# Performance work log

Hardware: AMD Instinct MI355X
Metric: run time of the kernel (lower is better)

Reference implementation:

```python
import jax, jax.numpy as jnp
import numpy as np

B, S, D, H = 2, 2048, 1024, 16
DK = D // H


def setup_inputs() -> dict:
    key = jax.random.key(0)
    ks = jax.random.split(key, 11)
    scale = 1.0 / np.sqrt(D)
    inp = {
        "query": jax.random.normal(ks[0], (B, S, D), dtype=jnp.float32),
        "key": jax.random.normal(ks[1], (B, S, D), dtype=jnp.float32),
        "value": jax.random.normal(ks[2], (B, S, D), dtype=jnp.float32),
        "Wq": jax.random.normal(ks[3], (D, D), dtype=jnp.float32) * scale,
        "bq": jnp.zeros((D,), dtype=jnp.float32),
        "Wk": jax.random.normal(ks[4], (D, D), dtype=jnp.float32) * scale,
        "bk": jnp.zeros((D,), dtype=jnp.float32),
        "Wv": jax.random.normal(ks[5], (D, D), dtype=jnp.float32) * scale,
        "bv": jnp.zeros((D,), dtype=jnp.float32),
        "Wo": jax.random.normal(ks[6], (D, D), dtype=jnp.float32) * scale,
        "bo": jnp.zeros((D,), dtype=jnp.float32),
    }
    return inp


def _split_heads(x):
    # [B,S,D] -> [B,H,S,DK]
    b, s, _ = x.shape
    return x.reshape(b, s, H, DK).transpose(0, 2, 1, 3)


def reference(query, key, value, Wq, bq, Wk, bk, Wv, bv, Wo, bo):
    q = _split_heads(query @ Wq.T + bq)
    k = _split_heads(key @ Wk.T + bk)
    v = _split_heads(value @ Wv.T + bv)
    # scaled dot-product attention: [B,H,S,S]
    scores = jnp.einsum("bhqd,bhkd->bhqk", q, k) / np.sqrt(DK).astype(np.float32)
    attn = jax.nn.softmax(scores, axis=-1)  # stable max-subtract softmax, same math
    ctx = jnp.einsum("bhqk,bhkd->bhqd", attn, v)  # [B,H,S,DK]
    ctx = ctx.transpose(0, 2, 1, 3).reshape(query.shape[0], -1, H * DK)
    return ctx @ Wo.T + bo
```

## Files before the change

### kernel.cpp

```cpp
#include <hip/hip_runtime.h>
#include <math.h>

constexpr int NB = 2;
constexpr int NS = 2048;
constexpr int ND = 1024;
constexpr int NH = 16;
constexpr int NDK = 64;

typedef __attribute__((ext_vector_type(8))) short short8;
typedef __attribute__((ext_vector_type(4))) float floatx4;

__device__ inline unsigned short f2bf(float x) {
    unsigned u = __builtin_bit_cast(unsigned, x);
    u += 0x7fffu + ((u >> 16) & 1u);
    return (unsigned short)(u >> 16);
}

__device__ inline uint4 pack8(float4 a, float4 b) {
    unsigned short t[8] = {f2bf(a.x), f2bf(a.y), f2bf(a.z), f2bf(a.w),
                           f2bf(b.x), f2bf(b.y), f2bf(b.z), f2bf(b.w)};
    return *(uint4*)t;
}

#define GLOAD_LDS16(g, l) __builtin_amdgcn_global_load_lds( \
    (const __attribute__((address_space(1))) void*)(g),     \
    (__attribute__((address_space(3))) void*)(l), 16, 0, 0)

#define QSCALE 0.18033688f

__global__ __launch_bounds__(256) void cvt_all(
    const float* __restrict__ s0, const float* __restrict__ s1,
    const float* __restrict__ s2, const float* __restrict__ s3,
    const float* __restrict__ s4, const float* __restrict__ s5,
    const float* __restrict__ s6,
    unsigned short* __restrict__ d0, unsigned short* __restrict__ d1,
    unsigned short* __restrict__ d2, unsigned short* __restrict__ d3,
    unsigned short* __restrict__ d4, unsigned short* __restrict__ d5,
    unsigned short* __restrict__ d6)
{
    const int y = blockIdx.y;
    const float* srcs[7] = {s0, s1, s2, s3, s4, s5, s6};
    unsigned short* dsts[7] = {d0, d1, d2, d3, d4, d5, d6};
    const int nel = (y < 3) ? NB * NS * ND : ND * ND;
    int i = (blockIdx.x * 256 + threadIdx.x) * 8;
    if (i >= nel) return;
    const float* s = srcs[y];
    unsigned short* d = dsts[y];
    float4 a = *(const float4*)(s + i);
    float4 b = *(const float4*)(s + i + 4);
    *(uint4*)(d + i) = pack8(a, b);
}

template<int QA, int QB>
__device__ __forceinline__ void mfma_quad(
    floatx4 (&acc)[8][4], const short8 (&ta)[4][2], const short8 (&tb)[2][2][2])
{
#pragma unroll
    for (int ii = 0; ii < 4; ++ii)
#pragma unroll
        for (int jj = 0; jj < 2; ++jj) {
            acc[QA * 4 + ii][QB * 2 + jj] = __builtin_amdgcn_mfma_f32_16x16x32_bf16(
                ta[ii][0], tb[QB][jj][0], acc[QA * 4 + ii][QB * 2 + jj], 0, 0, 0);
            acc[QA * 4 + ii][QB * 2 + jj] = __builtin_amdgcn_mfma_f32_16x16x32_bf16(
                ta[ii][1], tb[QB][jj][1], acc[QA * 4 + ii][QB * 2 + jj], 0, 0, 0);
        }
}

__global__ __launch_bounds__(512, 2) void gemm_qkv(
    const unsigned short* __restrict__ Xq, const unsigned short* __restrict__ Xk,
    const unsigned short* __restrict__ Xv,
    const unsigned short* __restrict__ Wq, const unsigned short* __restrict__ Wk,
    const unsigned short* __restrict__ Wv,
    const float* __restrict__ bq, const float* __restrict__ bk,
    const float* __restrict__ bv,
    unsigned short* __restrict__ Cq, unsigned short* __restrict__ Ck,
    unsigned short* __restrict__ Cv)
{
    __shared__ unsigned short As[2][256 * 64];
    __shared__ unsigned short Bs[2][256 * 64];

    const int tid = threadIdx.x, w = tid >> 6, lane = tid & 63;
    const int lo = lane & 15, quad = lane >> 4;
    const int bid = blockIdx.x;
    const int seg = bid >> 6;
    const int idx = bid & 63;
    const int xcd = idx & 7;
    const int t8  = idx >> 3;
    const int K = ND;

    int bm, bn;
    const unsigned short *A, *Bw;
    const float* bias;
    if (seg == 2) {
        bm = t8 & 3; bn = (t8 >> 2) * 8 + xcd;
        A = Wv; Bw = Xv; bias = bv;
    } else {
        bn = t8 & 3; bm = (t8 >> 2) * 8 + xcd;
        if (seg == 1) { A = Xk; Bw = Wk; bias = bk; }
        else          { A = Xq; Bw = Wq; bias = bq; }
    }

    const int WM = (w >> 2) * 128, WN = (w & 3) * 64;

    const int srow = tid >> 3;
    const int sgo  = ((tid & 7) ^ (srow & 7)) * 8;
    const unsigned short* Asrc = A  + (size_t)(bm * 256 + srow) * K + sgo;
    const unsigned short* Bsrc = Bw + (size_t)(bn * 256 + srow) * K + sgo;

#define SA(bf_, t_, s_) GLOAD_LDS16(Asrc + (size_t)(s_) * 64 * K + (t_) * 64, \
                                    &As[bf_][(s_) * 4096 + tid * 8])
#define SB(bf_, t_, s_) GLOAD_LDS16(Bsrc + (size_t)(s_) * 64 * K + (t_) * 64, \
                                    &Bs[bf_][(s_) * 4096 + tid * 8])

    const int rp0 = ((quad) ^ (lo & 7)) * 8;
    const int rp1 = ((4 + quad) ^ (lo & 7)) * 8;

    short8 ta[4][2], tb[2][2][2];

#define RDA(bf_, qa_) { _Pragma("unroll") \
    for (int ii = 0; ii < 4; ++ii) { \
        const unsigned short* p_ = &As[bf_][(WM + (qa_) * 64 + ii * 16 + lo) * 64]; \
        ta[ii][0] = *(const short8*)(p_ + rp0); \
        ta[ii][1] = *(const short8*)(p_ + rp1); } }
#define RDB(bf_, qb_) { _Pragma("unroll") \
    for (int jj = 0; jj < 2; ++jj) { \
        const unsigned short* p_ = &Bs[bf_][(WN + (qb_) * 32 + jj * 16 + lo) * 64]; \
        tb[qb_][jj][0] = *(const short8*)(p_ + rp0); \
        tb[qb_][jj][1] = *(const short8*)(p_ + rp1); } }

#define PH_SYNC1 __builtin_amdgcn_s_barrier(); \
    asm volatile("s_waitcnt lgkmcnt(0)" ::: "memory"); \
    __builtin_amdgcn_sched_barrier(0); \
    __builtin_amdgcn_s_setprio(1);
#define PH_SYNC2 __builtin_amdgcn_s_setprio(0); \
    __builtin_amdgcn_sched_barrier(0); \
    __builtin_amdgcn_s_barrier();

    floatx4 acc[8][4];
#pragma unroll
    for (int i = 0; i < 8; ++i)
#pragma unroll
        for (int j = 0; j < 4; ++j) acc[i][j] = (floatx4){0.f, 0.f, 0.f, 0.f};

    SB(0, 0, 0); SB(0, 0, 1); SB(0, 0, 2); SB(0, 0, 3);
    SA(0, 0, 0); SA(0, 0, 1); SA(0, 0, 2); SA(0, 0, 3);
    SB(1, 1, 0); SB(1, 1, 1); SB(1, 1, 2); SB(1, 1, 3);
    asm volatile("s_waitcnt vmcnt(4)" ::: "memory");
    __builtin_amdgcn_s_barrier();

    constexpr int NIT = ND / 128;
#pragma unroll 1
    for (int it = 0; it < NIT; ++it) {
        const bool nl = (it < NIT - 1);
        const int t1 = 2 * it + 1, t2 = 2 * it + 2, t3 = 2 * it + 3;

        RDA(0, 0); RDB(0, 0);
        SA(1, t1, 0); SA(1, t1, 1);
        PH_SYNC1; mfma_quad<0, 0>(acc, ta, tb); PH_SYNC2;

        RDB(0, 1);
        SA(1, t1, 2); SA(1, t1, 3);
        PH_SYNC1; mfma_quad<0, 1>(acc, ta, tb); PH_SYNC2;

        RDA(0, 1);
        if (nl) { SB(0, t2, 0); SB(0, t2, 1); }
        PH_SYNC1; mfma_quad<1, 1>(acc, ta, tb); PH_SYNC2;

        if (nl) { SB(0, t2, 2); SB(0, t2, 3); }
        if (nl) asm volatile("s_waitcnt vmcnt(4)" ::: "memory");
        else    asm volatile("s_waitcnt vmcnt(0)" ::: "memory");
        PH_SYNC1; mfma_quad<1, 0>(acc, ta, tb); PH_SYNC2;

        RDA(1, 0); RDB(1, 0);
        if (nl) { SA(0, t2, 0); SA(0, t2, 1); }
        PH_SYNC1; mfma_quad<0, 0>(acc, ta, tb); PH_SYNC2;

        RDB(1, 1);
        if (nl) { SA(0, t2, 2); SA(0, t2, 3); }
        PH_SYNC1; mfma_quad<0, 1>(acc, ta, tb); PH_SYNC2;

        RDA(1, 1);
        if (nl) { SB(1, t3, 0); SB(1, t3, 1); }
        PH_SYNC1; mfma_quad<1, 1>(acc, ta, tb); PH_SYNC2;

        if (nl) { SB(1, t3, 2); SB(1, t3, 3); }
        if (nl) asm volatile("s_waitcnt vmcnt(4)" ::: "memory");
        PH_SYNC1; mfma_quad<1, 0>(acc, ta, tb); PH_SYNC2;
    }

#undef SA
#undef SB
#undef RDA
#undef RDB
#undef PH_SYNC1
#undef PH_SYNC2

    if (seg < 2) {
        unsigned short* C = seg ? Ck : Cq;
        const float scale = seg ? 1.f : QSCALE;
#pragma unroll
        for (int j = 0; j < 4; ++j) {
            const int col = bn * 256 + WN + j * 16 + lo;
            const float bb = bias[col];
#pragma unroll
            for (int i = 0; i < 8; ++i)
#pragma unroll
                for (int r = 0; r < 4; ++r) {
                    const int row = bm * 256 + WM + i * 16 + quad * 4 + r;
                    C[(size_t)row * ND + col] = f2bf((acc[i][j][r] + bb) * scale);
                }
        }
    } else {
#pragma unroll
        for (int i = 0; i < 8; ++i)
#pragma unroll
            for (int r = 0; r < 4; ++r) {
                const int row = bm * 256 + WM + i * 16 + quad * 4 + r;
                const float bb = bias[row];
#pragma unroll
                for (int j = 0; j < 4; ++j) {
                    const int col = bn * 256 + WN + j * 16 + lo;
                    const int b = col >> 11, s = col & (NS - 1);
                    Cv[(size_t)(b * ND + row) * NS + s] = f2bf(acc[i][j][r] + bb);
                }
            }
    }
}

constexpr int PRS = 72;

__global__ __launch_bounds__(512, 4) void attn_mfma(
    const unsigned short* __restrict__ qb,
    const unsigned short* __restrict__ kb,
    const unsigned short* __restrict__ vt,
    float* __restrict__ cacc0, float* __restrict__ cacc1,
    float* __restrict__ lbuf)
{
    __shared__ unsigned short Ks[2][64 * 64];
    __shared__ unsigned short Vs[2][64 * 64];
    __shared__ unsigned short Pt[8][32 * PRS];

    const int tid = threadIdx.x, w = tid >> 6, lane = tid & 63;
    const int lo = lane & 15, quad = lane >> 4;
    const int bid = blockIdx.x;
    const int xcd = bid & 7;
    const int tt  = bid >> 3;
    const int qgrp = tt & 7;
    const int bhk  = (tt >> 3) * 8 + xcd;
    const int bh = bhk >> 1, ksp = bhk & 1;
    const int b = bh >> 4, h = bh & 15;
    const int q0 = qgrp * 256 + w * 32;

    short8 qf[2][2];
    #pragma unroll
    for (int qt = 0; qt < 2; ++qt) {
        const unsigned short* qrow =
            qb + (size_t)(b * NS + q0 + qt * 16 + lo) * ND + h * NDK + quad * 8;
        qf[qt][0] = *(const short8*)(qrow);
        qf[qt][1] = *(const short8*)(qrow + 32);
    }

    const int r0 = tid >> 3, g0 = (tid & 7) ^ (r0 & 7);
    const unsigned short* Ksrc = kb + (size_t)(b * NS + r0) * ND + h * NDK + g0 * 8;
    const unsigned short* Vsrc = vt + (size_t)(bh * NDK + r0) * NS + g0 * 8;

#define STAGE(bf_, k_) { \
    GLOAD_LDS16(Ksrc + (size_t)(k_) * ND, &Ks[bf_][tid * 8]); \
    GLOAD_LDS16(Vsrc + (k_),              &Vs[bf_][tid * 8]); }

    floatx4 acc[2][4], lacc[2];
    #pragma unroll
    for (int qt = 0; qt < 2; ++qt) {
        lacc[qt] = (floatx4){0.f, 0.f, 0.f, 0.f};
        #pragma unroll
        for (int cb = 0; cb < 4; ++cb) acc[qt][cb] = (floatx4){0.f, 0.f, 0.f, 0.f};
    }

    const short8 ones = {0x3F80, 0x3F80, 0x3F80, 0x3F80,
                         0x3F80, 0x3F80, 0x3F80, 0x3F80};
    unsigned short* pw = &Pt[w][0];
    const int pos0 = (quad ^ (lo & 7)) * 8;
    const int pos1 = ((4 + quad) ^ (lo & 7)) * 8;

    const int kbase = ksp * 1024;
    STAGE(0, kbase);

    #pragma unroll 2
    for (int it = 0; it < 16; ++it) {
        const int bf = it & 1;
        if (it < 15) {
            STAGE(bf ^ 1, kbase + (it + 1) * 64);
            asm volatile("s_waitcnt vmcnt(2)" ::: "memory");
        } else {
            asm volatile("s_waitcnt vmcnt(0)" ::: "memory");
        }
        __builtin_amdgcn_s_barrier();
        __builtin_amdgcn_sched_barrier(0);

        const unsigned short* Kc = Ks[bf];
        const unsigned short* Vc = Vs[bf];

        floatx4 s[2][4];
        __builtin_amdgcn_s_setprio(1);
        #pragma unroll
        for (int t = 0; t < 4; ++t) {
            const int rw = (t * 16 + lo) * 64;
            const short8 kf0 = *(const short8*)(Kc + rw + pos0);
            const short8 kf1 = *(const short8*)(Kc + rw + pos1);
            #pragma unroll
            for (int qt = 0; qt < 2; ++qt) {
                s[qt][t] = __builtin_amdgcn_mfma_f32_16x16x32_bf16(
                    kf0, qf[qt][0], (floatx4){0.f, 0.f, 0.f, 0.f}, 0, 0, 0);
                s[qt][t] = __builtin_amdgcn_mfma_f32_16x16x32_bf16(
                    kf1, qf[qt][1], s[qt][t], 0, 0, 0);
            }
        }
        __builtin_amdgcn_s_setprio(0);

        #pragma unroll
        for (int qt = 0; qt < 2; ++qt)
            #pragma unroll
            for (int t = 0; t < 4; ++t) {
                unsigned u0 = __builtin_bit_cast(unsigned, __builtin_amdgcn_exp2f(s[qt][t][0]));
                unsigned u1 = __builtin_bit_cast(unsigned, __builtin_amdgcn_exp2f(s[qt][t][1]));
                unsigned u2 = __builtin_bit_cast(unsigned, __builtin_amdgcn_exp2f(s[qt][t][2]));
                unsigned u3 = __builtin_bit_cast(unsigned, __builtin_amdgcn_exp2f(s[qt][t][3]));
                uint2 pk = {(u0 >> 16) | (u1 & 0xFFFF0000u),
                            (u2 >> 16) | (u3 & 0xFFFF0000u)};
                *(uint2*)(pw + (qt * 16 + lo) * PRS + t * 16 + quad * 4) = pk;
            }

        short8 pf[2][2];
        #pragma unroll
        for (int qt = 0; qt < 2; ++qt) {
            pf[qt][0] = *(const short8*)(pw + (qt * 16 + lo) * PRS + quad * 8);
            pf[qt][1] = *(const short8*)(pw + (qt * 16 + lo) * PRS + 32 + quad * 8);
            lacc[qt] = __builtin_amdgcn_mfma_f32_16x16x32_bf16(pf[qt][0], ones, lacc[qt], 0, 0, 0);
            lacc[qt] = __builtin_amdgcn_mfma_f32_16x16x32_bf16(pf[qt][1], ones, lacc[qt], 0, 0, 0);
        }

        __builtin_amdgcn_s_setprio(1);
        #pragma unroll
        for (int cb = 0; cb < 4; ++cb) {
            const int rw = (cb * 16 + lo) * 64;
            const short8 vf0 = *(const short8*)(Vc + rw + pos0);
            const short8 vf1 = *(const short8*)(Vc + rw + pos1);
            #pragma unroll
            for (int qt = 0; qt < 2; ++qt) {
                acc[qt][cb] = __builtin_amdgcn_mfma_f32_16x16x32_bf16(pf[qt][0], vf0, acc[qt][cb], 0, 0, 0);
                acc[qt][cb] = __builtin_amdgcn_mfma_f32_16x16x32_bf16(pf[qt][1], vf1, acc[qt][cb], 0, 0, 0);
            }
        }
        __builtin_amdgcn_s_setprio(0);

        __builtin_amdgcn_sched_barrier(0);
        __builtin_amdgcn_s_barrier();
    }
#undef STAGE

    float* ca = ksp ? cacc1 : cacc0;
    float* lb = lbuf + (size_t)ksp * (NB * NH * NS);
    #pragma unroll
    for (int qt = 0; qt < 2; ++qt) {
        #pragma unroll
        for (int cb = 0; cb < 4; ++cb)
            #pragma unroll
            for (int r = 0; r < 4; ++r) {
                size_t off = (size_t)(b * NS + q0 + qt * 16 + quad * 4 + r) * ND
                           + h * NDK + cb * 16 + lo;
                ca[off] = acc[qt][cb][r];
            }
        if (lo == 0)
            #pragma unroll
            for (int r = 0; r < 4; ++r)
                lb[(size_t)bh * NS + q0 + qt * 16 + quad * 4 + r] = lacc[qt][r];
    }
}

__global__ __launch_bounds__(256) void gemm_o(
    const float* __restrict__ cacc0, const float* __restrict__ cacc1,
    const float* __restrict__ lbuf, const unsigned short* __restrict__ Bw,
    const float* __restrict__ bias, float* __restrict__ Cout)
{
    __shared__ unsigned short As[64 * 64];
    __shared__ unsigned short Bs[2][128 * 64];
    const int tid = threadIdx.x, w = tid >> 6, lane = tid & 63;
    const int lo = lane & 15, quad = lane >> 4;
    const int bid = blockIdx.x;
    const int xcd = bid & 7;
    const int tt  = bid >> 3;
    const int bn  = tt & 7;
    const int bm  = (tt >> 3) * 8 + xcd;
    const int K = ND;
    const int wm = (w >> 1) * 32, wn = (w & 1) * 64;
    const size_t LHALF = (size_t)NB * NH * NS;

    const int ar = tid >> 3;
    const int ag = (tid & 7) ^ (ar & 7);
    const int tok0 = bm * 64 + ar, tok1 = tok0 + 32;
    const float* A00 = cacc0 + (size_t)tok0 * ND + ag * 8;
    const float* A01 = cacc1 + (size_t)tok0 * ND + ag * 8;
    const float* A10 = cacc0 + (size_t)tok1 * ND + ag * 8;
    const float* A11 = cacc1 + (size_t)tok1 * ND + ag * 8;
    const size_t lb0 = (size_t)((tok0 >> 11) << 4) * NS + (tok0 & (NS - 1));
    const size_t lb1 = (size_t)((tok1 >> 11) << 4) * NS + (tok1 & (NS - 1));
    unsigned short* AsD0 = As + tid * 8;
    unsigned short* AsD1 = As + (tid + 256) * 8;

    const unsigned short* Bg[4];
    int bsoff[4];
    #pragma unroll
    for (int p = 0; p < 4; ++p) {
        int c = tid + 256 * p, r = c >> 3, g = (c & 7) ^ (r & 7);
        Bg[p] = Bw + (size_t)(bn * 128 + r) * K + g * 8;
        bsoff[p] = c * 8;
    }

    floatx4 acc[2][4];
    #pragma unroll
    for (int i = 0; i < 2; ++i)
        #pragma unroll
        for (int j = 0; j < 4; ++j) acc[i][j] = (floatx4){0.f, 0.f, 0.f, 0.f};

    #pragma unroll
    for (int p = 0; p < 4; ++p) GLOAD_LDS16(Bg[p], &Bs[0][bsoff[p]]);

    float4 ra[8];
    float lv0, lv1;
    ra[0] = *(const float4*)(A00);     ra[1] = *(const float4*)(A00 + 4);
    ra[2] = *(const float4*)(A01);     ra[3] = *(const float4*)(A01 + 4);
    ra[4] = *(const float4*)(A10);     ra[5] = *(const float4*)(A10 + 4);
    ra[6] = *(const float4*)(A11);     ra[7] = *(const float4*)(A11 + 4);
    lv0 = lbuf[lb0] + lbuf[lb0 + LHALF];
    lv1 = lbuf[lb1] + lbuf[lb1 + LHALF];

    #pragma unroll 1
    for (int t = 0; t < 16; ++t) {
        const int k0 = t * 64;
        const int cur = t & 1;
        if (t < 15) {
            #pragma unroll
            for (int p = 0; p < 4; ++p)
                GLOAD_LDS16(Bg[p] + k0 + 64, &Bs[cur ^ 1][bsoff[p]]);
        }
        const float inv0 = __builtin_amdgcn_rcpf(lv0);
        const float inv1 = __builtin_amdgcn_rcpf(lv1);
        if (t < 15) asm volatile("s_waitcnt vmcnt(4)" ::: "memory");
        else        asm volatile("s_waitcnt vmcnt(0)" ::: "memory");
        __builtin_amdgcn_s_barrier();
        __builtin_amdgcn_sched_barrier(0);

        {
            float4 s0 = {(ra[0].x + ra[2].x) * inv0, (ra[0].y + ra[2].y) * inv0,
                         (ra[0].z + ra[2].z) * inv0, (ra[0].w + ra[2].w) * inv0};
            float4 s1 = {(ra[1].x + ra[3].x) * inv0, (ra[1].y + ra[3].y) * inv0,
                         (ra[1].z + ra[3].z) * inv0, (ra[1].w + ra[3].w) * inv0};
            *(uint4*)AsD0 = pack8(s0, s1);
            float4 s2 = {(ra[4].x + ra[6].x) * inv1, (ra[4].y + ra[6].y) * inv1,
                         (ra[4].z + ra[6].z) * inv1, (ra[4].w + ra[6].w) * inv1};
            float4 s3 = {(ra[5].x + ra[7].x) * inv1, (ra[5].y + ra[7].y) * inv1,
                         (ra[5].z + ra[7].z) * inv1, (ra[5].w + ra[7].w) * inv1};
            *(uint4*)AsD1 = pack8(s2, s3);
        }

        if (t < 15) {
            const int kn = k0 + 64;
            ra[0] = *(const float4*)(A00 + kn); ra[1] = *(const float4*)(A00 + kn + 4);
            ra[2] = *(const float4*)(A01 + kn); ra[3] = *(const float4*)(A01 + kn + 4);
            ra[4] = *(const float4*)(A10 + kn); ra[5] = *(const float4*)(A10 + kn + 4);
            ra[6] = *(const float4*)(A11 + kn); ra[7] = *(const float4*)(A11 + kn + 4);
            const size_t hoff = (size_t)(kn >> 6) * NS;
            lv0 = lbuf[lb0 + hoff] + lbuf[lb0 + hoff + LHALF];
            lv1 = lbuf[lb1 + hoff] + lbuf[lb1 + hoff + LHALF];
        }

        asm volatile("s_waitcnt lgkmcnt(0)" ::: "memory");
        __builtin_amdgcn_sched_barrier(0);
        __builtin_amdgcn_s_barrier();

        __builtin_amdgcn_s_setprio(1);
        #pragma unroll
        for (int s = 0; s < 2; ++s) {
            const int pos = ((s * 4 + quad) ^ (lo & 7)) * 8;
            short8 af[2], bf[4];
            #pragma unroll
            for (int i = 0; i < 2; ++i)
                af[i] = *(const short8*)(As + (wm + i * 16 + lo) * 64 + pos);
            #pragma unroll
            for (int j = 0; j < 4; ++j)
                bf[j] = *(const short8*)(&Bs[cur][(wn + j * 16 + lo) * 64] + pos);
            #pragma unroll
            for (int i = 0; i < 2; ++i)
                #pragma unroll
                for (int j = 0; j < 4; ++j)
                    acc[i][j] = __builtin_amdgcn_mfma_f32_16x16x32_bf16(af[i], bf[j], acc[i][j], 0, 0, 0);
        }
        __builtin_amdgcn_s_setprio(0);
        __builtin_amdgcn_sched_barrier(0);
        __builtin_amdgcn_s_barrier();
    }

    #pragma unroll
    for (int j = 0; j < 4; ++j) {
        const int col = bn * 128 + wn + j * 16 + lo;
        const float bb = bias[col];
        #pragma unroll
        for (int i = 0; i < 2; ++i)
            #pragma unroll
            for (int r = 0; r < 4; ++r) {
                const int row = bm * 64 + wm + i * 16 + quad * 4 + r;
                Cout[(size_t)row * ND + col] = acc[i][j][r] + bb;
            }
    }
}

extern "C" void kernel_launch(void* const* d_in, const int* in_sizes, int n_in,
                              void* d_out, int out_size, void* d_ws, size_t ws_size,
                              hipStream_t stream)
{
    const float* query = (const float*)d_in[0];
    const float* key   = (const float*)d_in[1];
    const float* value = (const float*)d_in[2];
    const float* Wq    = (const float*)d_in[3];
    const float* bq    = (const float*)d_in[4];
    const float* Wk    = (const float*)d_in[5];
    const float* bk    = (const float*)d_in[6];
    const float* Wv    = (const float*)d_in[7];
    const float* bv    = (const float*)d_in[8];
    const float* Wo    = (const float*)d_in[9];
    const float* bo    = (const float*)d_in[10];
    float* out = (float*)d_out;

    const size_t n  = (size_t)NB * NS * ND;
    const size_t nw = (size_t)ND * ND;

    unsigned short* X0   = (unsigned short*)d_ws;
    unsigned short* X1   = X0 + n;
    unsigned short* X2   = X1 + n;
    unsigned short* W0   = X2 + n;
    unsigned short* W1   = W0 + nw;
    unsigned short* W2   = W1 + nw;
    unsigned short* W3   = W2 + nw;
    unsigned short* qbuf = W3 + nw;
    unsigned short* kbuf = qbuf + n;
    unsigned short* vtb  = kbuf + n;
    float* cacc1 = (float*)(vtb + n);
    float* lbuf  = cacc1 + n;
    float* cacc0 = (float*)X1;

    cvt_all<<<dim3((int)(n / 2048), 7), 256, 0, stream>>>(
        query, key, value, Wq, Wk, Wv, Wo, X0, X1, X2, W0, W1, W2, W3);

    gemm_qkv<<<192, 512, 0, stream>>>(X0, X1, X2, W0, W1, W2,
                                      bq, bk, bv, qbuf, kbuf, vtb);

    attn_mfma<<<512, 512, 0, stream>>>(qbuf, kbuf, vtb, cacc0, cacc1, lbuf);

    gemm_o<<<512, 256, 0, stream>>>(cacc0, cacc1, lbuf, W3, bo, out);
}
```

Before: 219.2 us.

## Triple-buffer K/V tiles with one barrier per iteration and swizzle P tile

Switches the attention K/V staging from double to triple buffering. The next-next tile is prefetched right after the barrier, which makes the trailing barrier unnecessary and halves the number of barriers per iteration. The padded P staging buffer (stride 72) is replaced by an unpadded 64-wide buffer with an XOR swizzle, to avoid LDS bank conflicts while using less shared memory. In exchange, LDS use for K/V goes up, which may limit occupancy at 4 blocks per CU, and the loop is no longer unrolled.

```diff
diff --git a/kernel.cpp b/kernel.cpp
--- a/kernel.cpp
+++ b/kernel.cpp
@@ -227,8 +227,6 @@
     }
 }
 
-constexpr int PRS = 72;
-
 __global__ __launch_bounds__(512, 4) void attn_mfma(
     const unsigned short* __restrict__ qb,
     const unsigned short* __restrict__ kb,
@@ -236,9 +234,9 @@
     float* __restrict__ cacc0, float* __restrict__ cacc1,
     float* __restrict__ lbuf)
 {
-    __shared__ unsigned short Ks[2][64 * 64];
-    __shared__ unsigned short Vs[2][64 * 64];
-    __shared__ unsigned short Pt[8][32 * PRS];
+    __shared__ unsigned short Ks[3][64 * 64];
+    __shared__ unsigned short Vs[3][64 * 64];
+    __shared__ unsigned short Pt[8][32 * 64];
 
     const int tid = threadIdx.x, w = tid >> 6, lane = tid & 63;
     const int lo = lane & 15, quad = lane >> 4;
@@ -263,10 +261,12 @@
     const int r0 = tid >> 3, g0 = (tid & 7) ^ (r0 & 7);
     const unsigned short* Ksrc = kb + (size_t)(b * NS + r0) * ND + h * NDK + g0 * 8;
     const unsigned short* Vsrc = vt + (size_t)(bh * NDK + r0) * NS + g0 * 8;
-
-#define STAGE(bf_, k_) { \
-    GLOAD_LDS16(Ksrc + (size_t)(k_) * ND, &Ks[bf_][tid * 8]); \
-    GLOAD_LDS16(Vsrc + (k_),              &Vs[bf_][tid * 8]); }
+    unsigned short* Ks0 = &Ks[0][0];
+    unsigned short* Vs0 = &Vs[0][0];
+
+#define STAGE(bi_, k_) { \
+    GLOAD_LDS16(Ksrc + (size_t)(k_) * ND, Ks0 + (bi_) * 4096 + tid * 8); \
+    GLOAD_LDS16(Vsrc + (k_),              Vs0 + (bi_) * 4096 + tid * 8); }
 
     floatx4 acc[2][4], lacc[2];
     #pragma unroll
@@ -281,24 +281,23 @@
     unsigned short* pw = &Pt[w][0];
     const int pos0 = (quad ^ (lo & 7)) * 8;
     const int pos1 = ((4 + quad) ^ (lo & 7)) * 8;
+    const int pxor = (lo & 7) << 3;
 
     const int kbase = ksp * 1024;
     STAGE(0, kbase);
-
-    #pragma unroll 2
+    STAGE(1, kbase + 64);
+
+    int rd = 0, wr = 2;
+    #pragma unroll 1
     for (int it = 0; it < 16; ++it) {
-        const int bf = it & 1;
-        if (it < 15) {
-            STAGE(bf ^ 1, kbase + (it + 1) * 64);
-            asm volatile("s_waitcnt vmcnt(2)" ::: "memory");
-        } else {
-            asm volatile("s_waitcnt vmcnt(0)" ::: "memory");
-        }
+        if (it < 15) asm volatile("s_waitcnt vmcnt(2)" ::: "memory");
+        else         asm volatile("s_waitcnt vmcnt(0)" ::: "memory");
         __builtin_amdgcn_s_barrier();
         __builtin_amdgcn_sched_barrier(0);
-
-        const unsigned short* Kc = Ks[bf];
-        const unsigned short* Vc = Vs[bf];
+        if (it < 14) STAGE(wr, kbase + (it + 2) * 64);
+
+        const unsigned short* Kc = Ks0 + rd * 4096;
+        const unsigned short* Vc = Vs0 + rd * 4096;
 
         floatx4 s[2][4];
         __builtin_amdgcn_s_setprio(1);
@@ -327,14 +326,14 @@
                 unsigned u3 = __builtin_bit_cast(unsigned, __builtin_amdgcn_exp2f(s[qt][t][3]));
                 uint2 pk = {(u0 >> 16) | (u1 & 0xFFFF0000u),
                             (u2 >> 16) | (u3 & 0xFFFF0000u)};
-                *(uint2*)(pw + (qt * 16 + lo) * PRS + t * 16 + quad * 4) = pk;
+                *(uint2*)(pw + (qt * 16 + lo) * 64 + ((t * 16 + quad * 4) ^ pxor)) = pk;
             }
 
         short8 pf[2][2];
         #pragma unroll
         for (int qt = 0; qt < 2; ++qt) {
-            pf[qt][0] = *(const short8*)(pw + (qt * 16 + lo) * PRS + quad * 8);
-            pf[qt][1] = *(const short8*)(pw + (qt * 16 + lo) * PRS + 32 + quad * 8);
+            pf[qt][0] = *(const short8*)(pw + (qt * 16 + lo) * 64 + pos0);
+            pf[qt][1] = *(const short8*)(pw + (qt * 16 + lo) * 64 + pos1);
             lacc[qt] = __builtin_amdgcn_mfma_f32_16x16x32_bf16(pf[qt][0], ones, lacc[qt], 0, 0, 0);
             lacc[qt] = __builtin_amdgcn_mfma_f32_16x16x32_bf16(pf[qt][1], ones, lacc[qt], 0, 0, 0);
         }
@@ -353,8 +352,8 @@
         }
         __builtin_amdgcn_s_setprio(0);
 
-        __builtin_amdgcn_sched_barrier(0);
-        __builtin_amdgcn_s_barrier();
+        rd = (rd == 2) ? 0 : rd + 1;
+        wr = (wr == 2) ? 0 : wr + 1;
     }
 #undef STAGE
 
```

New measurement: 217.7 us (median of 2 runs). Within noise of the previous version (-0.7%).

## Fuse fp32-to-bf16 conversion into QKV GEMM loads, drop separate convert pass

Applied to the files above, without the earlier changes.

The QKV projection GEMM now reads fp32 activations and weights directly from global memory into registers, converts them to bf16 and writes them into LDS. Previously a separate kernel converted all inputs to bf16 first, and the GEMM used async global-to-LDS loads. Only the Wo weight is still converted by a small standalone kernel. This removes one full read and write pass over the inputs and one kernel launch. In exchange the GEMM loads twice the bytes per tile, the stages sync on register loads instead of async LDS DMA, and register pressure rises.

```diff
diff --git a/kernel.cpp b/kernel.cpp
--- a/kernel.cpp
+++ b/kernel.cpp
@@ -28,24 +28,10 @@
 
 #define QSCALE 0.18033688f
 
-__global__ __launch_bounds__(256) void cvt_all(
-    const float* __restrict__ s0, const float* __restrict__ s1,
-    const float* __restrict__ s2, const float* __restrict__ s3,
-    const float* __restrict__ s4, const float* __restrict__ s5,
-    const float* __restrict__ s6,
-    unsigned short* __restrict__ d0, unsigned short* __restrict__ d1,
-    unsigned short* __restrict__ d2, unsigned short* __restrict__ d3,
-    unsigned short* __restrict__ d4, unsigned short* __restrict__ d5,
-    unsigned short* __restrict__ d6)
+__global__ __launch_bounds__(256) void cvt_w(
+    const float* __restrict__ s, unsigned short* __restrict__ d)
 {
-    const int y = blockIdx.y;
-    const float* srcs[7] = {s0, s1, s2, s3, s4, s5, s6};
-    unsigned short* dsts[7] = {d0, d1, d2, d3, d4, d5, d6};
-    const int nel = (y < 3) ? NB * NS * ND : ND * ND;
     int i = (blockIdx.x * 256 + threadIdx.x) * 8;
-    if (i >= nel) return;
-    const float* s = srcs[y];
-    unsigned short* d = dsts[y];
     float4 a = *(const float4*)(s + i);
     float4 b = *(const float4*)(s + i + 4);
     *(uint4*)(d + i) = pack8(a, b);
@@ -67,10 +53,10 @@
 }
 
 __global__ __launch_bounds__(512, 2) void gemm_qkv(
-    const unsigned short* __restrict__ Xq, const unsigned short* __restrict__ Xk,
-    const unsigned short* __restrict__ Xv,
-    const unsigned short* __restrict__ Wq, const unsigned short* __restrict__ Wk,
-    const unsigned short* __restrict__ Wv,
+    const float* __restrict__ Xq, const float* __restrict__ Xk,
+    const float* __restrict__ Xv,
+    const float* __restrict__ Wq, const float* __restrict__ Wk,
+    const float* __restrict__ Wv,
     const float* __restrict__ bq, const float* __restrict__ bk,
     const float* __restrict__ bv,
     unsigned short* __restrict__ Cq, unsigned short* __restrict__ Ck,
@@ -89,7 +75,7 @@
     const int K = ND;
 
     int bm, bn;
-    const unsigned short *A, *Bw;
+    const float *A, *Bw;
     const float* bias;
     if (seg == 2) {
         bm = t8 & 3; bn = (t8 >> 2) * 8 + xcd;
@@ -104,13 +90,15 @@
 
     const int srow = tid >> 3;
     const int sgo  = ((tid & 7) ^ (srow & 7)) * 8;
-    const unsigned short* Asrc = A  + (size_t)(bm * 256 + srow) * K + sgo;
-    const unsigned short* Bsrc = Bw + (size_t)(bn * 256 + srow) * K + sgo;
-
-#define SA(bf_, t_, s_) GLOAD_LDS16(Asrc + (size_t)(s_) * 64 * K + (t_) * 64, \
-                                    &As[bf_][(s_) * 4096 + tid * 8])
-#define SB(bf_, t_, s_) GLOAD_LDS16(Bsrc + (size_t)(s_) * 64 * K + (t_) * 64, \
-                                    &Bs[bf_][(s_) * 4096 + tid * 8])
+    const float* Asrc = A  + (size_t)(bm * 256 + srow) * K + sgo;
+    const float* Bsrc = Bw + (size_t)(bn * 256 + srow) * K + sgo;
+
+#define LDA(t_, s_, a_, b_) { const float* p_ = Asrc + (size_t)(s_) * 64 * K + (t_) * 64; \
+    a_ = *(const float4*)(p_); b_ = *(const float4*)(p_ + 4); }
+#define LDB(t_, s_, a_, b_) { const float* p_ = Bsrc + (size_t)(s_) * 64 * K + (t_) * 64; \
+    a_ = *(const float4*)(p_); b_ = *(const float4*)(p_ + 4); }
+#define WRA(bf_, s_, a_, b_) *(uint4*)(&As[bf_][(s_) * 4096 + tid * 8]) = pack8(a_, b_);
+#define WRB(bf_, s_, a_, b_) *(uint4*)(&Bs[bf_][(s_) * 4096 + tid * 8]) = pack8(a_, b_);
 
     const int rp0 = ((quad) ^ (lo & 7)) * 8;
     const int rp1 = ((4 + quad) ^ (lo & 7)) * 8;
@@ -128,11 +116,14 @@
         tb[qb_][jj][0] = *(const short8*)(p_ + rp0); \
         tb[qb_][jj][1] = *(const short8*)(p_ + rp1); } }
 
-#define PH_SYNC1 __builtin_amdgcn_s_barrier(); \
+#define PH_IN  __builtin_amdgcn_sched_barrier(0); \
+    __builtin_amdgcn_s_barrier(); \
     asm volatile("s_waitcnt lgkmcnt(0)" ::: "memory"); \
     __builtin_amdgcn_sched_barrier(0); \
     __builtin_amdgcn_s_setprio(1);
-#define PH_SYNC2 __builtin_amdgcn_s_setprio(0); \
+#define PH_MID __builtin_amdgcn_s_setprio(0); \
+    __builtin_amdgcn_sched_barrier(0);
+#define PH_OUT asm volatile("s_waitcnt lgkmcnt(0)" ::: "memory"); \
     __builtin_amdgcn_sched_barrier(0); \
     __builtin_amdgcn_s_barrier();
 
@@ -142,11 +133,17 @@
 #pragma unroll
         for (int j = 0; j < 4; ++j) acc[i][j] = (floatx4){0.f, 0.f, 0.f, 0.f};
 
-    SB(0, 0, 0); SB(0, 0, 1); SB(0, 0, 2); SB(0, 0, 3);
-    SA(0, 0, 0); SA(0, 0, 1); SA(0, 0, 2); SA(0, 0, 3);
-    SB(1, 1, 0); SB(1, 1, 1); SB(1, 1, 2); SB(1, 1, 3);
-    asm volatile("s_waitcnt vmcnt(4)" ::: "memory");
-    __builtin_amdgcn_s_barrier();
+    {
+        float4 f0, f1, f2, f3, f4, f5, f6, f7;
+        LDB(0, 0, f0, f1); LDB(0, 1, f2, f3); LDB(0, 2, f4, f5); LDB(0, 3, f6, f7);
+        WRB(0, 0, f0, f1); WRB(0, 1, f2, f3); WRB(0, 2, f4, f5); WRB(0, 3, f6, f7);
+        LDA(0, 0, f0, f1); LDA(0, 1, f2, f3); LDA(0, 2, f4, f5); LDA(0, 3, f6, f7);
+        WRA(0, 0, f0, f1); WRA(0, 1, f2, f3); WRA(0, 2, f4, f5); WRA(0, 3, f6, f7);
+        LDB(1, 0, f0, f1); LDB(1, 1, f2, f3); LDB(1, 2, f4, f5); LDB(1, 3, f6, f7);
+        WRB(1, 0, f0, f1); WRB(1, 1, f2, f3); WRB(1, 2, f4, f5); WRB(1, 3, f6, f7);
+        asm volatile("s_waitcnt lgkmcnt(0)" ::: "memory");
+        __builtin_amdgcn_s_barrier();
+    }
 
     constexpr int NIT = ND / 128;
 #pragma unroll 1
@@ -154,46 +151,79 @@
         const bool nl = (it < NIT - 1);
         const int t1 = 2 * it + 1, t2 = 2 * it + 2, t3 = 2 * it + 3;
 
-        RDA(0, 0); RDB(0, 0);
-        SA(1, t1, 0); SA(1, t1, 1);
-        PH_SYNC1; mfma_quad<0, 0>(acc, ta, tb); PH_SYNC2;
-
-        RDB(0, 1);
-        SA(1, t1, 2); SA(1, t1, 3);
-        PH_SYNC1; mfma_quad<0, 1>(acc, ta, tb); PH_SYNC2;
-
-        RDA(0, 1);
-        if (nl) { SB(0, t2, 0); SB(0, t2, 1); }
-        PH_SYNC1; mfma_quad<1, 1>(acc, ta, tb); PH_SYNC2;
-
-        if (nl) { SB(0, t2, 2); SB(0, t2, 3); }
-        if (nl) asm volatile("s_waitcnt vmcnt(4)" ::: "memory");
-        else    asm volatile("s_waitcnt vmcnt(0)" ::: "memory");
-        PH_SYNC1; mfma_quad<1, 0>(acc, ta, tb); PH_SYNC2;
-
-        RDA(1, 0); RDB(1, 0);
-        if (nl) { SA(0, t2, 0); SA(0, t2, 1); }
-        PH_SYNC1; mfma_quad<0, 0>(acc, ta, tb); PH_SYNC2;
-
-        RDB(1, 1);
-        if (nl) { SA(0, t2, 2); SA(0, t2, 3); }
-        PH_SYNC1; mfma_quad<0, 1>(acc, ta, tb); PH_SYNC2;
-
-        RDA(1, 1);
-        if (nl) { SB(1, t3, 0); SB(1, t3, 1); }
-        PH_SYNC1; mfma_quad<1, 1>(acc, ta, tb); PH_SYNC2;
-
-        if (nl) { SB(1, t3, 2); SB(1, t3, 3); }
-        if (nl) asm volatile("s_waitcnt vmcnt(4)" ::: "memory");
-        PH_SYNC1; mfma_quad<1, 0>(acc, ta, tb); PH_SYNC2;
-    }
-
-#undef SA
-#undef SB
+        {
+            float4 f0, f1, f2, f3;
+            RDA(0, 0); RDB(0, 0);
+            LDA(t1, 0, f0, f1); LDA(t1, 1, f2, f3);
+            PH_IN; mfma_quad<0, 0>(acc, ta, tb); PH_MID;
+            WRA(1, 0, f0, f1); WRA(1, 1, f2, f3);
+            PH_OUT;
+        }
+        {
+            float4 f0, f1, f2, f3;
+            RDB(0, 1);
+            LDA(t1, 2, f0, f1); LDA(t1, 3, f2, f3);
+            PH_IN; mfma_quad<0, 1>(acc, ta, tb); PH_MID;
+            WRA(1, 2, f0, f1); WRA(1, 3, f2, f3);
+            PH_OUT;
+        }
+        {
+            float4 f0, f1, f2, f3;
+            RDA(0, 1);
+            if (nl) { LDB(t2, 0, f0, f1); LDB(t2, 1, f2, f3); }
+            PH_IN; mfma_quad<1, 1>(acc, ta, tb); PH_MID;
+            if (nl) { WRB(0, 0, f0, f1); WRB(0, 1, f2, f3); }
+            PH_OUT;
+        }
+        {
+            float4 f0, f1, f2, f3;
+            if (nl) { LDB(t2, 2, f0, f1); LDB(t2, 3, f2, f3); }
+            PH_IN; mfma_quad<1, 0>(acc, ta, tb); PH_MID;
+            if (nl) { WRB(0, 2, f0, f1); WRB(0, 3, f2, f3); }
+            PH_OUT;
+        }
+        {
+            float4 f0, f1, f2, f3;
+            RDA(1, 0); RDB(1, 0);
+            if (nl) { LDA(t2, 0, f0, f1); LDA(t2, 1, f2, f3); }
+            PH_IN; mfma_quad<0, 0>(acc, ta, tb); PH_MID;
+            if (nl) { WRA(0, 0, f0, f1); WRA(0, 1, f2, f3); }
+            PH_OUT;
+        }
+        {
+            float4 f0, f1, f2, f3;
+            RDB(1, 1);
+            if (nl) { LDA(t2, 2, f0, f1); LDA(t2, 3, f2, f3); }
+            PH_IN; mfma_quad<0, 1>(acc, ta, tb); PH_MID;
+            if (nl) { WRA(0, 2, f0, f1); WRA(0, 3, f2, f3); }
+            PH_OUT;
+        }
+        {
+            float4 f0, f1, f2, f3;
+            RDA(1, 1);
+            if (nl) { LDB(t3, 0, f0, f1); LDB(t3, 1, f2, f3); }
+            PH_IN; mfma_quad<1, 1>(acc, ta, tb); PH_MID;
+            if (nl) { WRB(1, 0, f0, f1); WRB(1, 1, f2, f3); }
+            PH_OUT;
+        }
+        {
+            float4 f0, f1, f2, f3;
+            if (nl) { LDB(t3, 2, f0, f1); LDB(t3, 3, f2, f3); }
+            PH_IN; mfma_quad<1, 0>(acc, ta, tb); PH_MID;
+            if (nl) { WRB(1, 2, f0, f1); WRB(1, 3, f2, f3); }
+            PH_OUT;
+        }
+    }
+
+#undef LDA
+#undef LDB
+#undef WRA
+#undef WRB
 #undef RDA
 #undef RDB
-#undef PH_SYNC1
-#undef PH_SYNC2
+#undef PH_IN
+#undef PH_MID
+#undef PH_OUT
 
     if (seg < 2) {
         unsigned short* C = seg ? Ck : Cq;
@@ -548,10 +578,9 @@
     float* lbuf  = cacc1 + n;
     float* cacc0 = (float*)X1;
 
-    cvt_all<<<dim3((int)(n / 2048), 7), 256, 0, stream>>>(
-        query, key, value, Wq, Wk, Wv, Wo, X0, X1, X2, W0, W1, W2, W3);
-
-    gemm_qkv<<<192, 512, 0, stream>>>(X0, X1, X2, W0, W1, W2,
+    cvt_w<<<512, 256, 0, stream>>>(Wo, W3);
+
+    gemm_qkv<<<192, 512, 0, stream>>>(query, key, value, Wq, Wk, Wv,
                                       bq, bk, bv, qbuf, kbuf, vtb);
 
     attn_mfma<<<512, 512, 0, stream>>>(qbuf, kbuf, vtb, cacc0, cacc1, lbuf);
```

Measured after the change: 397.4 us. +81.3%, slower.

## Halve attention query tile per wave and double grid with XOR-swizzled P buffer

Applied to the files above, without the earlier changes.

Each wave of the attention kernel now handles 16 query rows instead of 32, so a block covers 128 queries and the grid doubles to 1024 blocks. The P staging buffer drops its padded stride for an XOR swizzle, and launch bounds ask for 6 blocks per CU. The aim is more parallelism and occupancy through lower register and LDS use. In exchange, each K/V tile loaded into LDS is reused by half as many queries, so K/V global traffic doubles.

```diff
diff --git a/kernel.cpp b/kernel.cpp
--- a/kernel.cpp
+++ b/kernel.cpp
@@ -227,9 +227,7 @@
     }
 }
 
-constexpr int PRS = 72;
-
-__global__ __launch_bounds__(512, 4) void attn_mfma(
+__global__ __launch_bounds__(512, 6) void attn_mfma(
     const unsigned short* __restrict__ qb,
     const unsigned short* __restrict__ kb,
     const unsigned short* __restrict__ vt,
@@ -238,26 +236,25 @@
 {
     __shared__ unsigned short Ks[2][64 * 64];
     __shared__ unsigned short Vs[2][64 * 64];
-    __shared__ unsigned short Pt[8][32 * PRS];
+    __shared__ unsigned short Pt[8][16 * 64];
 
     const int tid = threadIdx.x, w = tid >> 6, lane = tid & 63;
     const int lo = lane & 15, quad = lane >> 4;
     const int bid = blockIdx.x;
     const int xcd = bid & 7;
     const int tt  = bid >> 3;
-    const int qgrp = tt & 7;
-    const int bhk  = (tt >> 3) * 8 + xcd;
+    const int qgrp = tt & 15;
+    const int bhk  = (tt >> 4) * 8 + xcd;
     const int bh = bhk >> 1, ksp = bhk & 1;
     const int b = bh >> 4, h = bh & 15;
-    const int q0 = qgrp * 256 + w * 32;
-
-    short8 qf[2][2];
-    #pragma unroll
-    for (int qt = 0; qt < 2; ++qt) {
+    const int q0 = qgrp * 128 + w * 16;
+
+    short8 qf0, qf1;
+    {
         const unsigned short* qrow =
-            qb + (size_t)(b * NS + q0 + qt * 16 + lo) * ND + h * NDK + quad * 8;
-        qf[qt][0] = *(const short8*)(qrow);
-        qf[qt][1] = *(const short8*)(qrow + 32);
+            qb + (size_t)(b * NS + q0 + lo) * ND + h * NDK + quad * 8;
+        qf0 = *(const short8*)(qrow);
+        qf1 = *(const short8*)(qrow + 32);
     }
 
     const int r0 = tid >> 3, g0 = (tid & 7) ^ (r0 & 7);
@@ -268,19 +265,17 @@
     GLOAD_LDS16(Ksrc + (size_t)(k_) * ND, &Ks[bf_][tid * 8]); \
     GLOAD_LDS16(Vsrc + (k_),              &Vs[bf_][tid * 8]); }
 
-    floatx4 acc[2][4], lacc[2];
+    floatx4 acc[4], lacc;
+    lacc = (floatx4){0.f, 0.f, 0.f, 0.f};
     #pragma unroll
-    for (int qt = 0; qt < 2; ++qt) {
-        lacc[qt] = (floatx4){0.f, 0.f, 0.f, 0.f};
-        #pragma unroll
-        for (int cb = 0; cb < 4; ++cb) acc[qt][cb] = (floatx4){0.f, 0.f, 0.f, 0.f};
-    }
+    for (int cb = 0; cb < 4; ++cb) acc[cb] = (floatx4){0.f, 0.f, 0.f, 0.f};
 
     const short8 ones = {0x3F80, 0x3F80, 0x3F80, 0x3F80,
                          0x3F80, 0x3F80, 0x3F80, 0x3F80};
     unsigned short* pw = &Pt[w][0];
     const int pos0 = (quad ^ (lo & 7)) * 8;
     const int pos1 = ((4 + quad) ^ (lo & 7)) * 8;
+    const int pxor = (lo & 7) << 3;
 
     const int kbase = ksp * 1024;
     STAGE(0, kbase);
@@ -300,44 +295,36 @@
         const unsigned short* Kc = Ks[bf];
         const unsigned short* Vc = Vs[bf];
 
-        floatx4 s[2][4];
+        floatx4 s[4];
         __builtin_amdgcn_s_setprio(1);
         #pragma unroll
         for (int t = 0; t < 4; ++t) {
             const int rw = (t * 16 + lo) * 64;
             const short8 kf0 = *(const short8*)(Kc + rw + pos0);
             const short8 kf1 = *(const short8*)(Kc + rw + pos1);
-            #pragma unroll
-            for (int qt = 0; qt < 2; ++qt) {
-                s[qt][t] = __builtin_amdgcn_mfma_f32_16x16x32_bf16(
-                    kf0, qf[qt][0], (floatx4){0.f, 0.f, 0.f, 0.f}, 0, 0, 0);
-                s[qt][t] = __builtin_amdgcn_mfma_f32_16x16x32_bf16(
-                    kf1, qf[qt][1], s[qt][t], 0, 0, 0);
-            }
+            s[t] = __builtin_amdgcn_mfma_f32_16x16x32_bf16(
+                kf0, qf0, (floatx4){0.f, 0.f, 0.f, 0.f}, 0, 0, 0);
+            s[t] = __builtin_amdgcn_mfma_f32_16x16x32_bf16(
+                kf1, qf1, s[t], 0, 0, 0);
         }
         __builtin_amdgcn_s_setprio(0);
 
         #pragma unroll
-        for (int qt = 0; qt < 2; ++qt)
-            #pragma unroll
-            for (int t = 0; t < 4; ++t) {
-                unsigned u0 = __builtin_bit_cast(unsigned, __builtin_amdgcn_exp2f(s[qt][t][0]));
-                unsigned u1 = __builtin_bit_cast(unsigned, __builtin_amdgcn_exp2f(s[qt][t][1]));
-                unsigned u2 = __builtin_bit_cast(unsigned, __builtin_amdgcn_exp2f(s[qt][t][2]));
-                unsigned u3 = __builtin_bit_cast(unsigned, __builtin_amdgcn_exp2f(s[qt][t][3]));
-                uint2 pk = {(u0 >> 16) | (u1 & 0xFFFF0000u),
-                            (u2 >> 16) | (u3 & 0xFFFF0000u)};
-                *(uint2*)(pw + (qt * 16 + lo) * PRS + t * 16 + quad * 4) = pk;
-            }
-
-        short8 pf[2][2];
-        #pragma unroll
-        for (int qt = 0; qt < 2; ++qt) {
-            pf[qt][0] = *(const short8*)(pw + (qt * 16 + lo) * PRS + quad * 8);
-            pf[qt][1] = *(const short8*)(pw + (qt * 16 + lo) * PRS + 32 + quad * 8);
-            lacc[qt] = __builtin_amdgcn_mfma_f32_16x16x32_bf16(pf[qt][0], ones, lacc[qt], 0, 0, 0);
-            lacc[qt] = __builtin_amdgcn_mfma_f32_16x16x32_bf16(pf[qt][1], ones, lacc[qt], 0, 0, 0);
-        }
+        for (int t = 0; t < 4; ++t) {
+            unsigned u0 = __builtin_bit_cast(unsigned, __builtin_amdgcn_exp2f(s[t][0]));
+            unsigned u1 = __builtin_bit_cast(unsigned, __builtin_amdgcn_exp2f(s[t][1]));
+            unsigned u2 = __builtin_bit_cast(unsigned, __builtin_amdgcn_exp2f(s[t][2]));
+            unsigned u3 = __builtin_bit_cast(unsigned, __builtin_amdgcn_exp2f(s[t][3]));
+            uint2 pk = {(u0 >> 16) | (u1 & 0xFFFF0000u),
+                        (u2 >> 16) | (u3 & 0xFFFF0000u)};
+            *(uint2*)(pw + lo * 64 + ((t * 16 + quad * 4) ^ pxor)) = pk;
+        }
+
+        short8 pf0, pf1;
+        pf0 = *(const short8*)(pw + lo * 64 + pos0);
+        pf1 = *(const short8*)(pw + lo * 64 + pos1);
+        lacc = __builtin_amdgcn_mfma_f32_16x16x32_bf16(pf0, ones, lacc, 0, 0, 0);
+        lacc = __builtin_amdgcn_mfma_f32_16x16x32_bf16(pf1, ones, lacc, 0, 0, 0);
 
         __builtin_amdgcn_s_setprio(1);
         #pragma unroll
@@ -345,11 +332,8 @@
             const int rw = (cb * 16 + lo) * 64;
             const short8 vf0 = *(const short8*)(Vc + rw + pos0);
             const short8 vf1 = *(const short8*)(Vc + rw + pos1);
-            #pragma unroll
-            for (int qt = 0; qt < 2; ++qt) {
-                acc[qt][cb] = __builtin_amdgcn_mfma_f32_16x16x32_bf16(pf[qt][0], vf0, acc[qt][cb], 0, 0, 0);
-                acc[qt][cb] = __builtin_amdgcn_mfma_f32_16x16x32_bf16(pf[qt][1], vf1, acc[qt][cb], 0, 0, 0);
-            }
+            acc[cb] = __builtin_amdgcn_mfma_f32_16x16x32_bf16(pf0, vf0, acc[cb], 0, 0, 0);
+            acc[cb] = __builtin_amdgcn_mfma_f32_16x16x32_bf16(pf1, vf1, acc[cb], 0, 0, 0);
         }
         __builtin_amdgcn_s_setprio(0);
 
@@ -361,20 +345,17 @@
     float* ca = ksp ? cacc1 : cacc0;
     float* lb = lbuf + (size_t)ksp * (NB * NH * NS);
     #pragma unroll
-    for (int qt = 0; qt < 2; ++qt) {
-        #pragma unroll
-        for (int cb = 0; cb < 4; ++cb)
-            #pragma unroll
-            for (int r = 0; r < 4; ++r) {
-                size_t off = (size_t)(b * NS + q0 + qt * 16 + quad * 4 + r) * ND
-                           + h * NDK + cb * 16 + lo;
-                ca[off] = acc[qt][cb][r];
-            }
-        if (lo == 0)
-            #pragma unroll
-            for (int r = 0; r < 4; ++r)
-                lb[(size_t)bh * NS + q0 + qt * 16 + quad * 4 + r] = lacc[qt][r];
-    }
+    for (int cb = 0; cb < 4; ++cb)
+        #pragma unroll
+        for (int r = 0; r < 4; ++r) {
+            size_t off = (size_t)(b * NS + q0 + quad * 4 + r) * ND
+                       + h * NDK + cb * 16 + lo;
+            ca[off] = acc[cb][r];
+        }
+    if (lo == 0)
+        #pragma unroll
+        for (int r = 0; r < 4; ++r)
+            lb[(size_t)bh * NS + q0 + quad * 4 + r] = lacc[r];
 }
 
 __global__ __launch_bounds__(256) void gemm_o(
@@ -554,7 +535,7 @@
     gemm_qkv<<<192, 512, 0, stream>>>(X0, X1, X2, W0, W1, W2,
                                       bq, bk, bv, qbuf, kbuf, vtb);
 
-    attn_mfma<<<512, 512, 0, stream>>>(qbuf, kbuf, vtb, cacc0, cacc1, lbuf);
+    attn_mfma<<<1024, 512, 0, stream>>>(qbuf, kbuf, vtb, cacc0, cacc1, lbuf);
 
     gemm_o<<<512, 256, 0, stream>>>(cacc0, cacc1, lbuf, W3, bo, out);
 }
```

After: 227.4 us. 3.7% more time.
